# Optimization experiments

Hardware: AMD Instinct MI355X
Metric: run time of the kernel (lower is better)

The kernel has to match this reference:

```python
import jax, jax.numpy as jnp
import numpy as np

B, S, H = 64, 256, 768


def _lstm_cell(x, h, c, Wih, Whh, b):
    # PyTorch LSTMCell gate order: i, f, g, o
    g = x @ Wih.T + h @ Whh.T + b
    i, f, gg, o = jnp.split(g, 4, axis=-1)
    c = jax.nn.sigmoid(f) * c + jax.nn.sigmoid(i) * jnp.tanh(gg)
    h = jax.nn.sigmoid(o) * jnp.tanh(c)
    return h, c


def _bilstm(x, Wih_f, Whh_f, b_f, Wih_b, Whh_b, b_b):
    Bb, Ss, D = x.shape
    Hh = Whh_f.shape[1]

    def scan_dir(xs, Wih, Whh, b):
        def step(carry, x_t):
            h, c = carry
            h, c = _lstm_cell(x_t, h, c, Wih, Whh, b)
            return (h, c), h
        init = (jnp.zeros((Bb, Hh), x.dtype), jnp.zeros((Bb, Hh), x.dtype))
        _, hs = jax.lax.scan(step, init, xs)
        return hs

    xt = jnp.swapaxes(x, 0, 1)                      # [S, B, D]
    hf = scan_dir(xt, Wih_f, Whh_f, b_f)            # [S, B, H]
    hb = scan_dir(xt[::-1], Wih_b, Whh_b, b_b)[::-1]
    return jnp.swapaxes(jnp.concatenate([hf, hb], -1), 0, 1)  # [B, S, 2H]


def _decode(lstm_out, golds, subw_Wih, subw_Whh, subw_b,
            word_Wih, word_Whh, word_b, cls_W, cls_b):
    Bb, Ss, D = lstm_out.shape
    Hh = subw_Whh.shape[1]
    bidx = jnp.arange(Bb)
    subw_map = jnp.array([1, 2, 2], dtype=jnp.int32)   # subword_action_map
    word_map = jnp.array([0, 1, 1], dtype=jnp.int32)   # word_action_map

    sh = jnp.zeros((Bb, 2 * Ss + 2, Hh), lstm_out.dtype)  # subword stack (h)
    sc = jnp.zeros((Bb, 2 * Ss + 2, Hh), lstm_out.dtype)  # subword stack (c)
    wh = jnp.zeros((Bb, Ss + 1, Hh), lstm_out.dtype)       # word stack (h)
    wc = jnp.zeros((Bb, Ss + 1, Hh), lstm_out.dtype)       # word stack (c)
    sp = jnp.zeros((Bb,), jnp.int32)
    wp = jnp.zeros((Bb,), jnp.int32)

    xt = jnp.swapaxes(lstm_out, 0, 1)  # [S, B, 2H]
    gt = jnp.swapaxes(golds, 0, 1).astype(jnp.int32)
    xs = (xt[:-1], xt[1:], gt[1:])     # idx = 1..S-1

    def step(carry, inputs):
        sh, sc, sp, wh, wc, wp = carry
        x_prev, x_cur, g = inputs
        # subword stack LSTM: read top, push new state at pos+1
        h1, c1 = _lstm_cell(x_prev, sh[bidx, sp], sc[bidx, sp], subw_Wih, subw_Whh, subw_b)
        sh = sh.at[bidx, sp + 1].set(h1)
        sc = sc.at[bidx, sp + 1].set(c1)
        subword = jnp.concatenate([h1, c1], axis=-1)   # [B, 2H]
        # word stack LSTM
        wh1, wc1 = _lstm_cell(subword, wh[bidx, wp], wc[bidx, wp], word_Wih, word_Whh, word_b)
        wh = wh.at[bidx, wp + 1].set(wh1)
        wc = wc.at[bidx, wp + 1].set(wc1)
        out = jnp.concatenate([wh1, x_cur], axis=-1) @ cls_W.T + cls_b  # [B, 2]
        # training path: pos updates driven by gold actions
        sp = sp + subw_map[g]
        wp = wp + word_map[g]
        return (sh, sc, sp, wh, wc, wp), out

    _, outs = jax.lax.scan(step, (sh, sc, sp, wh, wc, wp), xs)  # [S-1, B, 2]
    first = jnp.broadcast_to(jnp.array([-1.0, 1.0], lstm_out.dtype), (Bb, 1, 2))
    return jnp.concatenate([first, jnp.swapaxes(outs, 0, 1)], axis=1)  # [B, S, 2]


def setup_inputs() -> dict:
    key = jax.random.key(0)
    ks = jax.random.split(key, 16)
    w = lambda k, shp: jax.random.normal(k, shp, dtype=jnp.float32) * 0.02
    return {
        "hidden_state": jax.random.normal(ks[0], (B, S, H), dtype=jnp.float32),
        "golds": jax.random.randint(ks[1], (B, S), 0, 2, dtype=jnp.int32),
        "lstm_Wih_f": w(ks[2], (4 * H, H)),
        "lstm_Whh_f": w(ks[3], (4 * H, H)),
        "lstm_b_f": w(ks[4], (4 * H,)),
        "lstm_Wih_b": w(ks[5], (4 * H, H)),
        "lstm_Whh_b": w(ks[6], (4 * H, H)),
        "lstm_b_b": w(ks[7], (4 * H,)),
        "subw_Wih": w(ks[8], (4 * H, 2 * H)),
        "subw_Whh": w(ks[9], (4 * H, H)),
        "subw_b": w(ks[10], (4 * H,)),
        "word_Wih": w(ks[11], (4 * H, 2 * H)),
        "word_Whh": w(ks[12], (4 * H, H)),
        "word_b": w(ks[13], (4 * H,)),
        "cls_W": w(ks[14], (2, 3 * H)),
        "cls_b": w(ks[15], (2,)),
    }


def reference(hidden_state, lstm_Wih_f, lstm_Whh_f, lstm_b_f,
              lstm_Wih_b, lstm_Whh_b, lstm_b_b,
              subw_Wih, subw_Whh, subw_b,
              word_Wih, word_Whh, word_b,
              cls_W, cls_b, golds):
    lstm_out = _bilstm(hidden_state, lstm_Wih_f, lstm_Whh_f, lstm_b_f,
                       lstm_Wih_b, lstm_Whh_b, lstm_b_b)
    return _decode(lstm_out, golds, subw_Wih, subw_Whh, subw_b,
                   word_Wih, word_Whh, word_b, cls_W, cls_b)
```

## Files before the change

kernel.cpp:

```cpp
#include <hip/hip_runtime.h>

#define B_  64
#define S_  256
#define H_  768
#define H4_ 3072
#define D2_ 1536
#define SEG 64
#define USZ (64*2304)

using u16 = unsigned short;
using u32 = unsigned int;
using u64 = unsigned long long;
typedef __attribute__((ext_vector_type(8))) short bf16x8;
typedef __attribute__((ext_vector_type(4))) float f32x4;
typedef __attribute__((ext_vector_type(4))) unsigned int u32x4;

#define DEV __device__ __forceinline__

DEV float bf2f(u16 u){ union{u32 i; float f;} c; c.i = ((u32)u)<<16; return c.f; }
DEV u16 f2bf(float f){ union{float f; u32 i;} c; c.f = f; return (u16)((c.i + 0x7FFFu + ((c.i>>16)&1u)) >> 16); }
DEV float sigm(float x){ return 1.f/(1.f + __expf(-x)); }
DEV float tanh_(float x){ return 2.f/(1.f + __expf(-2.f*x)) - 1.f; }

DEV void astore32(u16* p, u32 v){ __hip_atomic_store((u32*)p, v, __ATOMIC_RELAXED, __HIP_MEMORY_SCOPE_AGENT); }
DEV int afload(const int* p){ return __hip_atomic_load(p, __ATOMIC_RELAXED, __HIP_MEMORY_SCOPE_AGENT); }

DEV f32x4 mfma16(bf16x8 a, bf16x8 b, f32x4 c){
  return __builtin_amdgcn_mfma_f32_16x16x32_bf16(a, b, c, 0, 0, 0);
}

DEV void llc_load96(const u16* p, u32x4& a0, u32x4& a1, u32x4& a2,
                    u32x4& a3, u32x4& a4, u32x4& a5){
  asm volatile(
    "global_load_dwordx4 %0, %6, off sc0 sc1\n\t"
    "global_load_dwordx4 %1, %6, off offset:16 sc0 sc1\n\t"
    "global_load_dwordx4 %2, %6, off offset:32 sc0 sc1\n\t"
    "global_load_dwordx4 %3, %6, off offset:48 sc0 sc1\n\t"
    "global_load_dwordx4 %4, %6, off offset:64 sc0 sc1\n\t"
    "global_load_dwordx4 %5, %6, off offset:80 sc0 sc1\n\t"
    "s_waitcnt vmcnt(0)"
    : "=&v"(a0), "=&v"(a1), "=&v"(a2), "=&v"(a3), "=&v"(a4), "=&v"(a5)
    : "v"(p));
}
DEV void stage48llc(u16* dst, const u16* src){
  u32x4 a0,a1,a2,a3,a4,a5;
  llc_load96(src, a0,a1,a2,a3,a4,a5);
  *(u32x4*)(dst)    = a0; *(u32x4*)(dst+8)  = a1;
  *(u32x4*)(dst+16) = a2; *(u32x4*)(dst+24) = a3;
  *(u32x4*)(dst+32) = a4; *(u32x4*)(dst+40) = a5;
}
DEV void stage48llcz(u16* dst, const u16* src, bool keep){
  u32x4 a0,a1,a2,a3,a4,a5;
  llc_load96(src, a0,a1,a2,a3,a4,a5);
  const u32x4 z = {0u,0u,0u,0u};
  if (!keep){ a0=z; a1=z; a2=z; a3=z; a4=z; a5=z; }
  *(u32x4*)(dst)    = a0; *(u32x4*)(dst+8)  = a1;
  *(u32x4*)(dst+16) = a2; *(u32x4*)(dst+24) = a3;
  *(u32x4*)(dst+32) = a4; *(u32x4*)(dst+40) = a5;
}

__global__ void k_conv(const float* __restrict__ src, u16* __restrict__ dst,
                       int cols, int sld, int dld){
  const long r = blockIdx.x;
  for (int c = threadIdx.x*4; c < cols; c += 1024) {
    const float* sp = src + r*sld + c;
    float a = sp[0], b = sp[1], cc = sp[2], d = sp[3];
    u64 pack = (u64)f2bf(a) | ((u64)f2bf(b)<<16) | ((u64)f2bf(cc)<<32) | ((u64)f2bf(d)<<48);
    *(u64*)(dst + r*dld + c) = pack;
  }
}

__global__ __launch_bounds__(256) void k_gemm(
    const u16* __restrict__ A, const u16* __restrict__ W,
    const float* __restrict__ bias, u16* __restrict__ C, int K, int t0)
{
  __shared__ u16 at[128*40];
  __shared__ u16 bt[128*40];
  const int tid = threadIdx.x;
  const int L = tid & 63, wv = tid >> 6;
  const int mq = wv >> 1, nq = wv & 1;
  const int l16 = L & 15, quad = L >> 4;
  const long mb = blockIdx.y, nb = blockIdx.x;

  f32x4 acc[4][4];
  #pragma unroll
  for (int m=0;m<4;++m)
    #pragma unroll
    for (int n=0;n<4;++n)
      acc[m][n] = (f32x4){0.f,0.f,0.f,0.f};

  const int r = tid >> 1, c0 = (tid & 1) * 16;
  const int fr = (int)mb*128 + r;
  const long arow = ((long)(fr >> 6))*S_ + t0 + (fr & 63);
  const u16* Arow = A + arow*(long)K + c0;
  const u16* Wrow = W + (nb*128 + r)*(long)K + c0;

  for (int kb = 0; kb < K; kb += 32) {
    *(u32x4*)&at[r*40 + c0]     = *(const u32x4*)(Arow + kb);
    *(u32x4*)&at[r*40 + c0 + 8] = *(const u32x4*)(Arow + kb + 8);
    *(u32x4*)&bt[r*40 + c0]     = *(const u32x4*)(Wrow + kb);
    *(u32x4*)&bt[r*40 + c0 + 8] = *(const u32x4*)(Wrow + kb + 8);
    __syncthreads();
    bf16x8 af[4], bfr[4];
    #pragma unroll
    for (int m=0;m<4;++m) af[m]  = *(const bf16x8*)&at[(mq*64 + m*16 + l16)*40 + quad*8];
    #pragma unroll
    for (int n=0;n<4;++n) bfr[n] = *(const bf16x8*)&bt[(nq*64 + n*16 + l16)*40 + quad*8];
    #pragma unroll
    for (int m=0;m<4;++m)
      #pragma unroll
      for (int n=0;n<4;++n)
        acc[m][n] = mfma16(af[m], bfr[n], acc[m][n]);
    __syncthreads();
  }
  #pragma unroll
  for (int n=0;n<4;++n) {
    const long col = nb*128 + nq*64 + n*16 + l16;
    const float bv = bias[col];
    #pragma unroll
    for (int m=0;m<4;++m) {
      const long row0 = mb*128 + mq*64 + m*16 + quad*4;
      #pragma unroll
      for (int rr=0;rr<4;++rr)
        C[(row0+rr)*3072 + col] = f2bf(acc[m][n][rr] + bv);
    }
  }
}

__global__ __launch_bounds__(512,2) void k_bilstm(
    const u16* __restrict__ Gf, const u16* __restrict__ Gb,
    const u16* __restrict__ Whhf, const u16* __restrict__ Whhb,
    const u16* __restrict__ h0, u16* __restrict__ lstm,
    float* __restrict__ cstf, float* __restrict__ cstb,
    int* __restrict__ flags, int t0f, int tb0, int ep0)
{
  __shared__ __align__(16) u16 lds[32*776];
  float* gbuf = (float*)lds;
  const int wg = blockIdx.x;
  const int dir = wg / 96, rem = wg % 96, mh = rem / 48, s = rem % 48;
  const int grp = dir*2 + mh;
  const int tid = threadIdx.x;
  const int wave = tid >> 6, q = wave & 3, kh = wave >> 2;
  const int L = tid & 63, l16 = L & 15, quad = L >> 4;
  const int srw = tid >> 4, scl = (tid & 15) * 48;

  const u16* Gsrc = dir ? Gb : Gf;
  const u16* W    = dir ? Whhb : Whhf;
  float* cst      = dir ? cstb : cstf;

  bf16x8 bfr[12];
  {
    const u16* wr = W + (long)(q*H_ + s*16 + l16)*H_ + kh*384 + quad*8;
    #pragma unroll
    for (int kk=0;kk<12;++kk) bfr[kk] = *(const bf16x8*)(wr + kk*32);
  }

  const int lb = tid >> 3, cdl = (tid & 7) * 2;
  const int eb = mh*32 + lb, col = s*16 + cdl;
  const bool ew = (tid < 256);
  float creg[2] = {0.f, 0.f};
  if (ew){ creg[0] = cst[eb*H_ + col]; creg[1] = cst[eb*H_ + col + 1]; }

  u32 g0=0,g1=0,g2=0,g3=0;
  if (ew){
    const int tp0 = dir ? (tb0 + SEG-1) : t0f;
    const int gidx = eb*SEG + (dir ? (tp0 - tb0) : (tp0 - t0f));
    const u16* grow = Gsrc + (long)gidx*H4_ + col;
    g0 = *(const u32*)(grow);      g1 = *(const u32*)(grow + H_);
    g2 = *(const u32*)(grow+2*H_); g3 = *(const u32*)(grow+3*H_);
  }

  for (int t=0; t<SEG; ++t) {
    const int tp = dir ? (tb0 + SEG-1 - t) : (t0f + t);
    const bool first = dir ? (tp == S_-1) : (tp == 0);
    const u16* hbase; long ldh;
    if (first){ hbase = h0 + dir*H_; ldh = D2_; }
    else {
      const int tprev = dir ? (tp+1) : (tp-1);
      hbase = lstm + (long)tprev*D2_ + dir*H_;
      ldh = (long)S_*D2_;
    }
    stage48llc(&lds[srw*776 + scl], hbase + (long)(mh*32 + srw)*ldh + scl);
    __syncthreads();
    f32x4 acc[2];
    acc[0] = (f32x4){0.f,0.f,0.f,0.f}; acc[1] = acc[0];
    #pragma unroll
    for (int kk=0;kk<12;++kk)
      #pragma unroll
      for (int m=0;m<2;++m){
        bf16x8 a = *(const bf16x8*)&lds[(m*16+l16)*776 + kh*384 + kk*32 + quad*8];
        acc[m] = mfma16(a, bfr[kk], acc[m]);
      }
    __syncthreads();
    #pragma unroll
    for (int m=0;m<2;++m)
      #pragma unroll
      for (int rr=0;rr<4;++rr)
        gbuf[(q*2+kh)*512 + (m*16+quad*4+rr)*16 + l16] = acc[m][rr];
    __syncthreads();
    if (ew){
      u32 gr[4] = {g0,g1,g2,g3};
      u32 hp = 0;
      #pragma unroll
      for (int i=0;i<2;++i){
        float gv[4];
        #pragma unroll
        for (int qq=0;qq<4;++qq)
          gv[qq] = gbuf[(qq*2+0)*512 + lb*16 + cdl+i]
                 + gbuf[(qq*2+1)*512 + lb*16 + cdl+i]
                 + bf2f((u16)(gr[qq] >> (16*i)));
        const float c = sigm(gv[1])*creg[i] + sigm(gv[0])*tanh_(gv[2]);
        creg[i] = c;
        const float h = sigm(gv[3])*tanh_(c);
        hp |= ((u32)f2bf(h)) << (16*i);
      }
      astore32(lstm + ((long)eb*S_ + tp)*D2_ + dir*H_ + col, hp);
    }
    __threadfence_block();
    __syncthreads();
    if (tid == 0)
      __hip_atomic_store(&flags[(grp*48 + s)*64], ep0 + t + 1, __ATOMIC_RELAXED, __HIP_MEMORY_SCOPE_AGENT);
    if (ew){
      const int t2 = t + 1;
      const int tp2 = dir ? (tb0 + SEG-1 - t2) : (t0f + t2);
      const long gidx2 = (long)eb*SEG + (dir ? (tp2 - tb0) : (tp2 - t0f));
      const u16* grow2 = Gsrc + gidx2*H4_ + col;
      g0 = *(const u32*)(grow2);      g1 = *(const u32*)(grow2 + H_);
      g2 = *(const u32*)(grow2+2*H_); g3 = *(const u32*)(grow2+3*H_);
    }
    if ((int)tid < 48) {
      while (afload(&flags[(grp*48 + (int)tid)*64]) < ep0 + t + 1)
        __builtin_amdgcn_s_sleep(1);
    }
    __syncthreads();
  }
  if (ew){ cst[eb*H_ + col] = creg[0]; cst[eb*H_ + col + 1] = creg[1]; }
}

__global__ __launch_bounds__(512,1) void k_decode(
    const u16* __restrict__ Gsub, const u16* __restrict__ Wsub,
    const u16* __restrict__ Wwrd, const float* __restrict__ wbias,
    const float* __restrict__ clsW, const int* __restrict__ golds,
    u16* __restrict__ U,
    float* __restrict__ scS, float* __restrict__ wcS, float* __restrict__ whS,
    float* __restrict__ partials, int* __restrict__ flags, int r0)
{
  __shared__ __align__(16) u16 ab[2][32*392];
  float* gbuf = (float*)ab;
  const int wg = blockIdx.x;
  const int role = wg / 96, rem = wg % 96, mh = rem / 48, s = rem % 48;
  const int grp = role*2 + mh;
  const int tid = threadIdx.x;
  const int wave = tid >> 6, q = wave & 3, kh = wave >> 2;
  const int L = tid & 63, l16 = L & 15, quad = L >> 4;
  const int su = tid & 255, srw = su >> 3, scl = (su & 7) * 48;
  const int srw0 = tid >> 4, scl0 = (tid & 15) * 48;
  const int lb = tid >> 3, cdl = (tid & 7)*2;
  const int eb = mh*32 + lb, col = s*16 + cdl;
  const bool ew = (tid < 256);
  const int sb  = mh*32 + srw;
  const int sb0 = mh*32 + srw0;
  u16* abf = &ab[0][0];

  bf16x8 wfr[36];
  float st0[2] = {0.f,0.f}, st1[2] = {0.f,0.f}, st2[2] = {0.f,0.f};
  float wbv[4][2], clv[2][2];
  if (role == 0){
    const u16* wr = Wsub + (long)(q*H_ + s*16 + l16)*H_ + kh*384 + quad*8;
    #pragma unroll
    for (int kk=0;kk<12;++kk) wfr[kk] = *(const bf16x8*)(wr + kk*32);
    if (ew){ st0[0] = scS[eb*H_+col]; st0[1] = scS[eb*H_+col+1]; }
  } else {
    const u16* wr = Wwrd + (long)(q*H_ + s*16 + l16)*2304 + kh*384 + quad*8;
    #pragma unroll
    for (int cc=0;cc<3;++cc)
      #pragma unroll
      for (int kk=0;kk<12;++kk)
        wfr[cc*12+kk] = *(const bf16x8*)(wr + cc*768 + kk*32);
    if (ew){
      st1[0] = wcS[eb*H_+col]; st1[1] = wcS[eb*H_+col+1];
      st2[0] = whS[eb*H_+col]; st2[1] = whS[eb*H_+col+1];
      #pragma unroll
      for (int qq=0;qq<4;++qq){ wbv[qq][0]=wbias[qq*H_+col]; wbv[qq][1]=wbias[qq*H_+col+1]; }
      clv[0][0]=clsW[col]; clv[0][1]=clsW[col+1];
      clv[1][0]=clsW[2304+col]; clv[1][1]=clsW[2304+col+1];
    }
  }

  int stg_g = golds[sb0*S_ + ((r0 < 255) ? r0 : 255)];

  for (int rr=0; rr<SEG; ++rr){
    const int r = r0 + rr;
    u32 g0=0,g1=0,g2=0,g3=0; int gld_e = 0, gld = 0;
    if (ew){
      if (role == 0 && r <= 254){
        gld_e = golds[eb*S_ + r + 1];
        const u16* grow = Gsub + ((long)eb*SEG + rr)*H4_ + col;
        g0 = *(const u32*)(grow);      g1 = *(const u32*)(grow + H_);
        g2 = *(const u32*)(grow+2*H_); g3 = *(const u32*)(grow+3*H_);
      } else if (role == 1 && r >= 1){
        gld = golds[eb*S_ + r];
      }
    }
    if (tid < 96){
      int idx, tgt;
      if (tid < 48){ idx = mh*48 + tid; tgt = r; }
      else { idx = (2+mh)*48 + (tid-48); tgt = (role==0) ? (r-6) : r; }
      while (afload(&flags[idx*64]) < tgt) __builtin_amdgcn_s_sleep(1);
    }
    __syncthreads();

    const u16* Uprev = U + ((r+7)&7)*(long)USZ;
    u16*       Ucur  = U + (r&7)*(long)USZ;

    if (role == 0){
      if (r <= 254){
        const bool keep_s = (r > 0) && (stg_g == 0);
        stage48llcz(&abf[srw0*776 + scl0], Uprev + (long)sb0*2304 + scl0, keep_s);
        __syncthreads();
        f32x4 acc[2];
        acc[0] = (f32x4){0.f,0.f,0.f,0.f}; acc[1] = acc[0];
        #pragma unroll
        for (int kk=0;kk<12;++kk)
          #pragma unroll
          for (int m=0;m<2;++m){
            bf16x8 a = *(const bf16x8*)&abf[(m*16+l16)*776 + kh*384 + kk*32 + quad*8];
            acc[m] = mfma16(a, wfr[kk], acc[m]);
          }
        __syncthreads();
        stg_g = golds[sb0*S_ + ((r+1 < 255) ? r+1 : 255)];
        #pragma unroll
        for (int m=0;m<2;++m)
          #pragma unroll
          for (int r4=0;r4<4;++r4)
            gbuf[(q*2+kh)*512 + (m*16+quad*4+r4)*16 + l16] = acc[m][r4];
        __syncthreads();
        if (ew){
          const bool keep = (gld_e == 0);
          u32 gr[4] = {g0,g1,g2,g3};
          u32 hp=0, cp=0;
          #pragma unroll
          for (int i=0;i<2;++i){
            float gv[4];
            #pragma unroll
            for (int qq=0;qq<4;++qq)
              gv[qq] = gbuf[(qq*2+0)*512 + lb*16 + cdl+i]
                     + gbuf[(qq*2+1)*512 + lb*16 + cdl+i]
                     + bf2f((u16)(gr[qq] >> (16*i)));
            const float c1 = sigm(gv[1])*st0[i] + sigm(gv[0])*tanh_(gv[2]);
            const float h1 = sigm(gv[3])*tanh_(c1);
            st0[i] = keep ? c1 : 0.f;
            hp |= ((u32)f2bf(h1)) << (16*i);
            cp |= ((u32)f2bf(c1)) << (16*i);
          }
          astore32(Ucur + (long)eb*2304 + col, hp);
          astore32(Ucur + (long)eb*2304 + H_ + col, cp);
        }
      }
    } else {
      if (r >= 1){
        const u16* urow = Uprev + (long)sb*2304;
        if (kh == 0){
          stage48llc(&ab[0][srw*392 + scl], urow + scl);
        }
        __syncthreads();
        f32x4 acc[2];
        acc[0] = (f32x4){0.f,0.f,0.f,0.f}; acc[1] = acc[0];
        #pragma unroll
        for (int p=0;p<6;++p){
          if ((p & 1) == kh){
            const int cc = p >> 1;
            #pragma unroll
            for (int kk=0;kk<12;++kk)
              #pragma unroll
              for (int m=0;m<2;++m){
                bf16x8 a = *(const bf16x8*)&ab[p&1][(m*16+l16)*392 + kk*32 + quad*8];
                acc[m] = mfma16(a, wfr[cc*12+kk], acc[m]);
              }
          } else if (p < 5){
            stage48llc(&ab[(p+1)&1][srw*392 + scl], urow + (p+1)*384 + scl);
          }
          __syncthreads();
        }
        #pragma unroll
        for (int m=0;m<2;++m)
          #pragma unroll
          for (int r4=0;r4<4;++r4)
            gbuf[(q*2+kh)*512 + (m*16+quad*4+r4)*16 + l16] = acc[m][r4];
        __syncthreads();
        if (ew){
          const bool keep = (gld == 0);
          const int tp = r - 1;
          float p0 = 0.f, p1 = 0.f;
          u32 wp = 0;
          #pragma unroll
          for (int i=0;i<2;++i){
            float gv[4];
            #pragma unroll
            for (int qq=0;qq<4;++qq)
              gv[qq] = gbuf[(qq*2+0)*512 + lb*16 + cdl+i]
                     + gbuf[(qq*2+1)*512 + lb*16 + cdl+i]
                     + wbv[qq][i];
            const float wc1 = sigm(gv[1])*st1[i] + sigm(gv[0])*tanh_(gv[2]);
            const float wh1 = sigm(gv[3])*tanh_(wc1);
            st1[i] = keep ? st1[i] : wc1;
            st2[i] = keep ? st2[i] : wh1;
            p0 += wh1 * clv[0][i];
            p1 += wh1 * clv[1][i];
            wp |= ((u32)f2bf(st2[i])) << (16*i);
          }
          astore32(Ucur + (long)eb*2304 + D2_ + col, wp);
          p0 += __shfl_xor(p0, 1); p0 += __shfl_xor(p0, 2); p0 += __shfl_xor(p0, 4);
          p1 += __shfl_xor(p1, 1); p1 += __shfl_xor(p1, 2); p1 += __shfl_xor(p1, 4);
          if ((tid & 7) == 0){
            float* pp = partials + ((long)(tp*48 + s)*64 + eb)*2;
            pp[0] = p0; pp[1] = p1;
          }
        }
      }
    }
    __threadfence_block();
    __syncthreads();
    if (tid == 0)
      __hip_atomic_store(&flags[(grp*48 + s)*64], r+1, __ATOMIC_RELAXED, __HIP_MEMORY_SCOPE_AGENT);
  }
  if (ew){
    if (role == 0){
      scS[eb*H_+col] = st0[0]; scS[eb*H_+col+1] = st0[1];
    } else {
      wcS[eb*H_+col] = st1[0]; wcS[eb*H_+col+1] = st1[1];
      whS[eb*H_+col] = st2[0]; whS[eb*H_+col+1] = st2[1];
    }
  }
}

__global__ __launch_bounds__(256) void k_cls(
    const u16* __restrict__ lstm, const float* __restrict__ partials,
    const float* __restrict__ clsW, const float* __restrict__ clsb,
    float* __restrict__ out)
{
  const int ts = blockIdx.x;
  const int b  = blockIdx.y;
  const int tid = threadIdx.x;
  if (ts == 0) {
    if (tid == 0) { out[(long)b*S_*2 + 0] = -1.f; out[(long)b*S_*2 + 1] = 1.f; }
    return;
  }
  const int t = ts - 1;
  float s0 = 0.f, s1 = 0.f;
  const u16* xr = lstm + ((long)b*S_ + ts)*D2_;
  for (int k = tid; k < D2_; k += 256) {
    const float xv = bf2f(xr[k]);
    s0 += xv * clsW[768 + k];
    s1 += xv * clsW[2304 + 768 + k];
  }
  if (tid < 48) {
    const float* pr = partials + ((long)(t*48 + tid)*64 + b)*2;
    s0 += pr[0]; s1 += pr[1];
  }
  __shared__ float r0[256], r1[256];
  r0[tid] = s0; r1[tid] = s1; __syncthreads();
  for (int off = 128; off > 0; off >>= 1) {
    if (tid < off) { r0[tid] += r0[tid+off]; r1[tid] += r1[tid+off]; }
    __syncthreads();
  }
  if (tid == 0) {
    out[((long)b*S_ + ts)*2 + 0] = r0[0] + clsb[0];
    out[((long)b*S_ + ts)*2 + 1] = r1[0] + clsb[1];
  }
}

extern "C" void kernel_launch(void* const* d_in, const int* in_sizes, int n_in,
                              void* d_out, int out_size, void* d_ws, size_t ws_size,
                              hipStream_t stream)
{
  (void)in_sizes; (void)n_in; (void)out_size; (void)ws_size;
  const float* x     = (const float*)d_in[0];
  const int*   golds = (const int*)d_in[1];
  const float* wihf  = (const float*)d_in[2];
  const float* whhf  = (const float*)d_in[3];
  const float* bfw   = (const float*)d_in[4];
  const float* wihb  = (const float*)d_in[5];
  const float* whhb  = (const float*)d_in[6];
  const float* bbw   = (const float*)d_in[7];
  const float* swih  = (const float*)d_in[8];
  const float* swhh  = (const float*)d_in[9];
  const float* sb    = (const float*)d_in[10];
  const float* wwih  = (const float*)d_in[11];
  const float* wwhh  = (const float*)d_in[12];
  const float* wb    = (const float*)d_in[13];
  const float* clsW  = (const float*)d_in[14];
  const float* clsb  = (const float*)d_in[15];
  float* out = (float*)d_out;

  char* base = (char*)d_ws;
  u16*   h0   = (u16*)(base + 0);
  int*   flg2 = (int*)(base + 1179648);
  int*   flg4 = (int*)(base + 1228800);
  float* cstf = (float*)(base + 1277952);
  float* cstb = (float*)(base + 1474560);
  float* scS  = (float*)(base + 1671168);
  float* wcS  = (float*)(base + 1867776);
  float* whS  = (float*)(base + 2064384);
  u16* xb     = (u16*)(base + 2260992);
  u16* wihf_b = (u16*)(base + 27426816);
  u16* whhf_b = (u16*)(base + 32145408);
  u16* wihb_b = (u16*)(base + 36864000);
  u16* whhb_b = (u16*)(base + 41582592);
  u16* swih_b = (u16*)(base + 46301184);
  u16* swhh_b = (u16*)(base + 55738368);
  u16* wwrd_b = (u16*)(base + 60456960);
  u16* Gfseg  = (u16*)(base + 74612736);
  u16* Gbseg  = (u16*)(base + 99778560);
  u16* lstm   = (u16*)(base + 124944384);
  u16* Gsubseg = Gfseg;
  float* prt   = (float*)Gbseg;
  u16* U       = (u16*)(base + 99778560 + 8388608);

  hipMemsetAsync(d_ws, 0, 2260992, stream);

  k_conv<<<16384, 256, 0, stream>>>(x,    xb,     768,  768,  768);
  k_conv<<<3072,  256, 0, stream>>>(wihf, wihf_b, 768,  768,  768);
  k_conv<<<3072,  256, 0, stream>>>(whhf, whhf_b, 768,  768,  768);
  k_conv<<<3072,  256, 0, stream>>>(wihb, wihb_b, 768,  768,  768);
  k_conv<<<3072,  256, 0, stream>>>(whhb, whhb_b, 768,  768,  768);
  k_conv<<<3072,  256, 0, stream>>>(swih, swih_b, 1536, 1536, 1536);
  k_conv<<<3072,  256, 0, stream>>>(swhh, swhh_b, 768,  768,  768);
  k_conv<<<3072,  256, 0, stream>>>(wwih, wwrd_b,        1536, 1536, 2304);
  k_conv<<<3072,  256, 0, stream>>>(wwhh, wwrd_b + 1536, 768,  768,  2304);

  dim3 gg(24, 32);
  for (int sgi = 0; sgi < 4; ++sgi) {
    const int t0f = sgi*SEG;
    const int tb0 = (3 - sgi)*SEG;
    k_gemm<<<gg, 256, 0, stream>>>(xb, wihf_b, bfw, Gfseg, 768, t0f);
    k_gemm<<<gg, 256, 0, stream>>>(xb, wihb_b, bbw, Gbseg, 768, tb0);
    k_bilstm<<<192, 512, 0, stream>>>(Gfseg, Gbseg, whhf_b, whhb_b, h0, lstm,
                                      cstf, cstb, flg2, t0f, tb0, sgi*SEG);
  }

  hipMemsetAsync(U, 0, 8*USZ*2, stream);

  for (int sgi = 0; sgi < 4; ++sgi) {
    const int r0 = sgi*SEG;
    k_gemm<<<gg, 256, 0, stream>>>(lstm, swih_b, sb, Gsubseg, 1536, r0);
    k_decode<<<192, 512, 0, stream>>>(Gsubseg, swhh_b, wwrd_b, wb, clsW, golds,
                                      U, scS, wcS, whS, prt, flg4, r0);
  }

  dim3 gc(256, 64);
  k_cls<<<gc, 256, 0, stream>>>(lstm, prt, clsW, clsb, out);
}
```

Measured before the change: 4.159 ms.

## Restage word-LSTM U loads into three full-width chunks with fewer barriers

The word-role decode step used to stage the previous U row in six 384-column pieces, alternating between two LDS buffers, with a barrier after each piece. Now all 512 threads load 768-column chunks into three LDS buffers. The first two chunks are loaded together, the third chunk's load is issued before the first MFMAs run, and the step uses three barriers instead of seven. The aim is to cut synchronisation and serial LDS staging latency on the sequential critical path, at the cost of more LDS (3x32x776 u16) and more live registers.

```diff
diff --git a/kernel.cpp b/kernel.cpp
--- a/kernel.cpp
+++ b/kernel.cpp
@@ -42,6 +42,20 @@
     : "=&v"(a0), "=&v"(a1), "=&v"(a2), "=&v"(a3), "=&v"(a4), "=&v"(a5)
     : "v"(p));
 }
+DEV void llc_load96_nw(const u16* p, u32x4& a0, u32x4& a1, u32x4& a2,
+                       u32x4& a3, u32x4& a4, u32x4& a5){
+  asm volatile(
+    "global_load_dwordx4 %0, %6, off sc0 sc1\n\t"
+    "global_load_dwordx4 %1, %6, off offset:16 sc0 sc1\n\t"
+    "global_load_dwordx4 %2, %6, off offset:32 sc0 sc1\n\t"
+    "global_load_dwordx4 %3, %6, off offset:48 sc0 sc1\n\t"
+    "global_load_dwordx4 %4, %6, off offset:64 sc0 sc1\n\t"
+    "global_load_dwordx4 %5, %6, off offset:80 sc0 sc1"
+    : "=&v"(a0), "=&v"(a1), "=&v"(a2), "=&v"(a3), "=&v"(a4), "=&v"(a5)
+    : "v"(p));
+}
+DEV void vmwait0(){ asm volatile("s_waitcnt vmcnt(0)" ::: "memory"); }
+
 DEV void stage48llc(u16* dst, const u16* src){
   u32x4 a0,a1,a2,a3,a4,a5;
   llc_load96(src, a0,a1,a2,a3,a4,a5);
@@ -57,6 +71,11 @@
   *(u32x4*)(dst)    = a0; *(u32x4*)(dst+8)  = a1;
   *(u32x4*)(dst+16) = a2; *(u32x4*)(dst+24) = a3;
   *(u32x4*)(dst+32) = a4; *(u32x4*)(dst+40) = a5;
+}
+DEV void wr48(u16* dst, const u32x4* a){
+  *(u32x4*)(dst)    = a[0]; *(u32x4*)(dst+8)  = a[1];
+  *(u32x4*)(dst+16) = a[2]; *(u32x4*)(dst+24) = a[3];
+  *(u32x4*)(dst+32) = a[4]; *(u32x4*)(dst+40) = a[5];
 }
 
 __global__ void k_conv(const float* __restrict__ src, u16* __restrict__ dst,
@@ -245,7 +264,7 @@
     float* __restrict__ scS, float* __restrict__ wcS, float* __restrict__ whS,
     float* __restrict__ partials, int* __restrict__ flags, int r0)
 {
-  __shared__ __align__(16) u16 ab[2][32*392];
+  __shared__ __align__(16) u16 ab[3][32*776];
   float* gbuf = (float*)ab;
   const int wg = blockIdx.x;
   const int role = wg / 96, rem = wg % 96, mh = rem / 48, s = rem % 48;
@@ -253,12 +272,10 @@
   const int tid = threadIdx.x;
   const int wave = tid >> 6, q = wave & 3, kh = wave >> 2;
   const int L = tid & 63, l16 = L & 15, quad = L >> 4;
-  const int su = tid & 255, srw = su >> 3, scl = (su & 7) * 48;
   const int srw0 = tid >> 4, scl0 = (tid & 15) * 48;
   const int lb = tid >> 3, cdl = (tid & 7)*2;
   const int eb = mh*32 + lb, col = s*16 + cdl;
   const bool ew = (tid < 256);
-  const int sb  = mh*32 + srw;
   const int sb0 = mh*32 + srw0;
   u16* abf = &ab[0][0];
 
@@ -359,29 +376,42 @@
       }
     } else {
       if (r >= 1){
-        const u16* urow = Uprev + (long)sb*2304;
-        if (kh == 0){
-          stage48llc(&ab[0][srw*392 + scl], urow + scl);
-        }
-        __syncthreads();
+        const u16* urow = Uprev + (long)sb0*2304;
+        u32x4 c0[6], c1[6], c2[6];
+        llc_load96_nw(urow + scl0,       c0[0],c0[1],c0[2],c0[3],c0[4],c0[5]);
+        llc_load96_nw(urow + 768 + scl0, c1[0],c1[1],c1[2],c1[3],c1[4],c1[5]);
+        vmwait0();
+        wr48(&ab[0][srw0*776 + scl0], c0);
+        wr48(&ab[1][srw0*776 + scl0], c1);
+        __syncthreads();
+        llc_load96_nw(urow + 1536 + scl0, c2[0],c2[1],c2[2],c2[3],c2[4],c2[5]);
         f32x4 acc[2];
         acc[0] = (f32x4){0.f,0.f,0.f,0.f}; acc[1] = acc[0];
         #pragma unroll
-        for (int p=0;p<6;++p){
-          if ((p & 1) == kh){
-            const int cc = p >> 1;
-            #pragma unroll
-            for (int kk=0;kk<12;++kk)
-              #pragma unroll
-              for (int m=0;m<2;++m){
-                bf16x8 a = *(const bf16x8*)&ab[p&1][(m*16+l16)*392 + kk*32 + quad*8];
-                acc[m] = mfma16(a, wfr[cc*12+kk], acc[m]);
-              }
-          } else if (p < 5){
-            stage48llc(&ab[(p+1)&1][srw*392 + scl], urow + (p+1)*384 + scl);
-          }
-          __syncthreads();
-        }
+        for (int kk=0;kk<12;++kk)
+          #pragma unroll
+          for (int m=0;m<2;++m){
+            bf16x8 a = *(const bf16x8*)&ab[0][(m*16+l16)*776 + kh*384 + kk*32 + quad*8];
+            acc[m] = mfma16(a, wfr[kk], acc[m]);
+          }
+        #pragma unroll
+        for (int kk=0;kk<12;++kk)
+          #pragma unroll
+          for (int m=0;m<2;++m){
+            bf16x8 a = *(const bf16x8*)&ab[1][(m*16+l16)*776 + kh*384 + kk*32 + quad*8];
+            acc[m] = mfma16(a, wfr[12+kk], acc[m]);
+          }
+        vmwait0();
+        wr48(&ab[2][srw0*776 + scl0], c2);
+        __syncthreads();
+        #pragma unroll
+        for (int kk=0;kk<12;++kk)
+          #pragma unroll
+          for (int m=0;m<2;++m){
+            bf16x8 a = *(const bf16x8*)&ab[2][(m*16+l16)*776 + kh*384 + kk*32 + quad*8];
+            acc[m] = mfma16(a, wfr[24+kk], acc[m]);
+          }
+        __syncthreads();
         #pragma unroll
         for (int m=0;m<2;++m)
           #pragma unroll
```

Result: no change. 4.131 ms (-0.7%).
